# Kernel optimization log

Measured on AMD Instinct MI355X. Metric: run time of the kernel, lower is better.

## Reference

```python
import jax, jax.numpy as jnp
import numpy as np
from jax import lax

B, C_KEY, H, W = 2, 512, 48, 48
HW = H * W
TOPK = 4


def _conv(x, w, b, pad):
    # x: NCHW, w: OIHW (torch Conv2d layout)
    y = lax.conv_general_dilated(x, w, (1, 1), [(pad, pad), (pad, pad)],
                                 dimension_numbers=('NCHW', 'OIHW', 'NCHW'))
    return y + b[None, :, None, None]


def _deconv(x, w, b, stride, pad):
    # torch ConvTranspose2d weight layout (in_c, out_c, kh, kw).
    # Equivalent dilated conv: flip kernel spatially, swap in/out,
    # lhs_dilation=stride, padding=k-1-p each side.
    k = w.shape[2]
    kern = jnp.transpose(jnp.flip(w, (2, 3)), (1, 0, 2, 3))  # OIHW
    y = lax.conv_general_dilated(x, kern, (1, 1),
                                 [(k - 1 - pad, k - 1 - pad)] * 2,
                                 lhs_dilation=(stride, stride),
                                 dimension_numbers=('NCHW', 'OIHW', 'NCHW'))
    return y + b[None, :, None, None]


def setup_inputs() -> dict:
    key = jax.random.key(0)
    ks = jax.random.split(key, 32)

    def nrm(i, shape, scale=1.0):
        return jax.random.normal(ks[i], shape, jnp.float32) * scale

    def unit_key(i):
        k_ = jax.random.normal(ks[i], (B, C_KEY, H, W), jnp.float32)
        return k_ / jnp.linalg.norm(k_, axis=1, keepdims=True)

    inp = {
        'feats_s16': nrm(0, (B, 1024, H, W)),
        'feats_s8': nrm(1, (B, 512, 2 * H, 2 * W)),
        'feats_s4': nrm(2, (B, 256, 4 * H, 4 * W)),
        'key': unit_key(3),
        'init_key': unit_key(4),
        'prev_key': unit_key(5),
        'init_seg_16': jax.random.uniform(ks[6], (B, 2, H, W), jnp.float32),
        'prev_seg_16': jax.random.uniform(ks[7], (B, 2, H, W), jnp.float32),
        'mask_feats': nrm(8, (B, 256, H, W), 0.1),
        # Decoder parameters (torch layouts)
        'w_conv1': nrm(9, (256, 1024, 1, 1), 0.03), 'b_conv1': jnp.zeros((256,), jnp.float32),
        'w_blend1': nrm(10, (256, 516, 3, 3), 0.02), 'b_blend1': jnp.zeros((256,), jnp.float32),
        'w_deconv1': nrm(11, (256, 2, 4, 4), 0.02), 'b_deconv1': jnp.zeros((2,), jnp.float32),
        'w_conv2': nrm(12, (256, 512, 1, 1), 0.04), 'b_conv2': jnp.zeros((256,), jnp.float32),
        'w_blend2': nrm(13, (256, 258, 3, 3), 0.02), 'b_blend2': jnp.zeros((256,), jnp.float32),
        'w_deconv2': nrm(14, (256, 2, 4, 4), 0.02), 'b_deconv2': jnp.zeros((2,), jnp.float32),
        'w_conv3': nrm(15, (256, 256, 1, 1), 0.06), 'b_conv3': jnp.zeros((256,), jnp.float32),
        'w_blend3': nrm(16, (256, 258, 3, 3), 0.02), 'b_blend3': jnp.zeros((256,), jnp.float32),
        'w_deconv3': nrm(17, (256, 2, 6, 6), 0.02), 'b_deconv3': jnp.zeros((2,), jnp.float32),
    }
    return inp


def _forward(feats_s16, feats_s8, feats_s4, key, init_key, prev_key,
             init_seg_16, prev_seg_16, mask_feats,
             w_conv1, b_conv1, w_blend1, b_blend1, w_deconv1, b_deconv1,
             w_conv2, b_conv2, w_blend2, b_blend2, w_deconv2, b_deconv2,
             w_conv3, b_conv3, w_blend3, b_blend3, w_deconv3, b_deconv3):
    relu = jax.nn.relu
    Bn, _, Hh, Ww = key.shape
    HWn = Hh * Ww

    kf = key.reshape(Bn, -1, HWn)
    # cosine similarities mapped to [0,1]; p = ref pixel, q = query pixel
    global_sim = (jnp.einsum('bcp,bcq->bpq', init_key.reshape(Bn, -1, HWn), kf) + 1.0) * 0.5
    local_sim = (jnp.einsum('bcp,bcq->bpq', prev_key.reshape(Bn, -1, HWn), kf) + 1.0) * 0.5

    def global_score(seg_ch):  # seg_ch: (B,H,W)
        s = global_sim * seg_ch.reshape(Bn, HWn, 1)
        return jnp.max(s, axis=1)  # (B,HW)

    def local_score(seg_ch):
        s = local_sim * seg_ch.reshape(Bn, HWn, 1)  # (B,HW,HW)
        cut = lax.top_k(s, TOPK)[0][..., -1:]       # kth-largest along key dim
        mn = jnp.min(s, axis=2, keepdims=True)
        s = jnp.where(s < cut, mn, s)               # threshold masking
        return jnp.max(s, axis=1)                   # (B,HW)

    matching_score = jnp.stack([
        global_score(init_seg_16[:, 0]),
        global_score(init_seg_16[:, 1]),
        local_score(prev_seg_16[:, 0]),
        local_score(prev_seg_16[:, 1]),
    ], axis=1).reshape(Bn, 4, Hh, Ww)

    # Decoder
    x = jnp.concatenate([relu(_conv(feats_s16, w_conv1, b_conv1, 0)),
                         matching_score, mask_feats], axis=1)
    s8 = _deconv(relu(_conv(x, w_blend1, b_blend1, 1)), w_deconv1, b_deconv1, 2, 1)
    x = jnp.concatenate([relu(_conv(feats_s8, w_conv2, b_conv2, 0)), s8], axis=1)
    s4 = _deconv(relu(_conv(x, w_blend2, b_blend2, 1)), w_deconv2, b_deconv2, 2, 1)
    x = jnp.concatenate([relu(_conv(feats_s4, w_conv3, b_conv3, 0)), s4], axis=1)
    final_score = _deconv(relu(_conv(x, w_blend3, b_blend3, 1)), w_deconv3, b_deconv3, 4, 1)
    return final_score


def reference(feats_s16, feats_s8, feats_s4, key, init_key, prev_key,
              init_seg_16, prev_seg_16, mask_feats,
              w_conv1, b_conv1, w_blend1, b_blend1, w_deconv1, b_deconv1,
              w_conv2, b_conv2, w_blend2, b_blend2, w_deconv2, b_deconv2,
              w_conv3, b_conv3, w_blend3, b_blend3, w_deconv3, b_deconv3):
    return _forward(feats_s16, feats_s8, feats_s4, key, init_key, prev_key,
                    init_seg_16, prev_seg_16, mask_feats,
                    w_conv1, b_conv1, w_blend1, b_blend1, w_deconv1, b_deconv1,
                    w_conv2, b_conv2, w_blend2, b_blend2, w_deconv2, b_deconv2,
                    w_conv3, b_conv3, w_blend3, b_blend3, w_deconv3, b_deconv3)
```

## Files before the change

kernel.cpp:

```cpp
#include <hip/hip_runtime.h>
#include <cstdio>

typedef unsigned short u16;
typedef __attribute__((ext_vector_type(4))) float f32x4;
typedef __attribute__((ext_vector_type(8))) short s16x8;
typedef __attribute__((ext_vector_type(4))) unsigned short u16x4;

#define DEV static __device__ __forceinline__

DEV float bf2f(u16 u) { union { unsigned int i; float f; } v; v.i = ((unsigned int)u) << 16; return v.f; }
DEV u16 f2bf(float f) {
  unsigned int x = __float_as_uint(f);
  unsigned int r = (x + 0x7fffu + ((x >> 16) & 1u)) >> 16;
  return (u16)r;
}

typedef const __attribute__((address_space(1))) unsigned int* gptr_t;
typedef __attribute__((address_space(3))) unsigned int* lptr_t;
DEV void gl16(const u16* g, u16* l) {
  __builtin_amdgcn_global_load_lds((gptr_t)g, (lptr_t)l, 16, 0, 0);
}

__global__ __launch_bounds__(256) void trans_key(const float* __restrict__ X,
    u16* __restrict__ Y)
{
  __shared__ u16 t[64][72];
  const int tid = threadIdx.x;
  const int n0 = blockIdx.x * 64, k0 = blockIdx.y * 64, b = blockIdx.z;
  const float* Xb = X + (size_t)b * 512 * 2304;
  const int nl = tid & 63, kr = tid >> 6;
#pragma unroll
  for (int kk = 0; kk < 16; ++kk) {
    int kl = kr + kk * 4;
    t[kl][nl] = f2bf(Xb[(size_t)(k0 + kl) * 2304 + n0 + nl]);
  }
  __syncthreads();
  const int nr = tid >> 2, kb = (tid & 3) * 16;
  u16* yp = Y + (size_t)b * 2304 * 512 + (size_t)(n0 + nr) * 512 + k0 + kb;
#pragma unroll
  for (int i = 0; i < 4; ++i) {
    u16x4 v;
#pragma unroll
    for (int e = 0; e < 4; ++e) v[e] = t[kb + i * 4 + e][nr];
    *(u16x4*)&yp[i * 4] = v;
  }
}

__global__ __launch_bounds__(256) void sim_gemm_128(const u16* __restrict__ AT,
    const u16* __restrict__ BT, u16* __restrict__ out)
{
  __shared__ alignas(16) u16 Al[2][8][64][8];
  __shared__ alignas(16) u16 Bl[2][8][64][8];
  const int tid = threadIdx.x;
  const int lane = tid & 63, wv = tid >> 6;
  const int fr = lane & 15, kq = lane >> 4;
  const int wr = wv >> 1, wc = wv & 1;
  const int n0 = blockIdx.x * 128, m0 = blockIdx.y * 128, b = blockIdx.z;
  const u16* Ab = AT + (size_t)b * 2304 * 512;
  const u16* Bb = BT + (size_t)b * 2304 * 512;
  const int ar0 = m0 + wv * 16 + fr, ar1 = m0 + (wv + 4) * 16 + fr;
  const int br0 = n0 + wv * 16 + fr, br1 = n0 + (wv + 4) * 16 + fr;
  f32x4 acc[4][4];
#pragma unroll
  for (int p = 0; p < 4; ++p)
#pragma unroll
    for (int j = 0; j < 4; ++j) acc[p][j] = (f32x4){0, 0, 0, 0};
  auto ISSUE = [&](int buf, int s) {
    const int k0 = s * 32 + kq * 8;
    gl16(&Ab[(size_t)ar0 * 512 + k0], &Al[buf][wv][0][0]);
    gl16(&Ab[(size_t)ar1 * 512 + k0], &Al[buf][wv + 4][0][0]);
    gl16(&Bb[(size_t)br0 * 512 + k0], &Bl[buf][wv][0][0]);
    gl16(&Bb[(size_t)br1 * 512 + k0], &Bl[buf][wv + 4][0][0]);
  };
  ISSUE(0, 0);
  __syncthreads();
  const int NS = 512 / 32;
  for (int s = 0; s < NS; ++s) {
    const int cur = s & 1;
    if (s + 1 < NS) ISSUE(cur ^ 1, s + 1);
    s16x8 bf[4], af[4];
#pragma unroll
    for (int j = 0; j < 4; ++j) bf[j] = *(const s16x8*)&Bl[cur][wc * 4 + j][lane][0];
#pragma unroll
    for (int p = 0; p < 4; ++p) af[p] = *(const s16x8*)&Al[cur][wr * 4 + p][lane][0];
#pragma unroll
    for (int p = 0; p < 4; ++p)
#pragma unroll
      for (int j = 0; j < 4; ++j)
        acc[p][j] = __builtin_amdgcn_mfma_f32_16x16x32_bf16(af[p], bf[j], acc[p][j], 0, 0, 0);
    __syncthreads();
  }
  const int col = lane & 15, rg = (lane >> 4) * 4;
#pragma unroll
  for (int p = 0; p < 4; ++p)
#pragma unroll
    for (int j = 0; j < 4; ++j)
#pragma unroll
      for (int r = 0; r < 4; ++r) {
        int pr = m0 + (wr * 4 + p) * 16 + rg + r;
        int q = n0 + (wc * 4 + j) * 16 + col;
        out[((size_t)b * 2304 + pr) * 2304 + q] = f2bf((acc[p][j][r] + 1.0f) * 0.5f);
      }
}

__global__ __launch_bounds__(256) void rowstats(const u16* __restrict__ simL,
    float* __restrict__ cutv, float* __restrict__ mnv)
{
  const int row = blockIdx.x;
  const int tid = threadIdx.x;
  const u16* r = simL + (size_t)row * 2304;
  float t0 = -1e30f, t1 = -1e30f, t2 = -1e30f, t3 = -1e30f, mn = 1e30f;
  for (int i = tid; i < 2304; i += 256) {
    float v = bf2f(r[i]);
    mn = fminf(mn, v);
    if (v > t3) {
      if (v > t2) { t3 = t2; if (v > t1) { t2 = t1; if (v > t0) { t1 = t0; t0 = v; } else t1 = v; } else t2 = v; }
      else t3 = v;
    }
  }
  __shared__ float s4[256][4];
  __shared__ float smv[256];
  s4[tid][0] = t0; s4[tid][1] = t1; s4[tid][2] = t2; s4[tid][3] = t3;
  smv[tid] = mn;
  __syncthreads();
  for (int s = 128; s > 0; s >>= 1) {
    if (tid < s) {
      float a0 = s4[tid][0], a1 = s4[tid][1], a2 = s4[tid][2], a3 = s4[tid][3];
      float b0 = s4[tid + s][0], b1 = s4[tid + s][1], b2 = s4[tid + s][2], b3 = s4[tid + s][3];
      float m0 = fmaxf(a0, b3), m1 = fmaxf(a1, b2), m2 = fmaxf(a2, b1), m3 = fmaxf(a3, b0);
      float c0 = fmaxf(m0, m2), c2 = fminf(m0, m2), c1 = fmaxf(m1, m3), c3 = fminf(m1, m3);
      s4[tid][0] = fmaxf(c0, c1); s4[tid][1] = fminf(c0, c1);
      s4[tid][2] = fmaxf(c2, c3); s4[tid][3] = fminf(c2, c3);
      smv[tid] = fminf(smv[tid], smv[tid + s]);
    }
    __syncthreads();
  }
  if (tid == 0) { cutv[row] = s4[0][3]; mnv[row] = smv[0]; }
}

__global__ __launch_bounds__(256) void zero_f(float* __restrict__ p, int n)
{
  int i = blockIdx.x * 256 + threadIdx.x;
  if (i < n) p[i] = 0.0f;
}

__global__ __launch_bounds__(256) void zero_u16v(u16* __restrict__ p, long n4)
{
  long i = (long)blockIdx.x * 256 + threadIdx.x;
  const long stride = (long)gridDim.x * 256;
  const uint2 z = {0u, 0u};
  for (; i < n4; i += stride) ((uint2*)p)[i] = z;
}

__global__ __launch_bounds__(256) void score_global(const u16* __restrict__ sim,
    const float* __restrict__ seg, float* __restrict__ msc, int chBase)
{
  const int b = blockIdx.z;
  const int q = blockIdx.x * 256 + threadIdx.x;
  const int p0 = blockIdx.y * 128;
  const u16* sp = sim + ((size_t)b * 2304 + p0) * 2304 + q;
  const float* sg = seg + (size_t)b * 2 * 2304;
  float m0 = 0.0f, m1 = 0.0f;
  for (int p = 0; p < 128; ++p) {
    float sv = bf2f(sp[(size_t)p * 2304]);
    float s0 = sg[p0 + p];
    float s1 = sg[2304 + p0 + p];
    m0 = fmaxf(m0, sv * s0);
    m1 = fmaxf(m1, sv * s1);
  }
  atomicMax((int*)&msc[((size_t)b * 4 + chBase) * 2304 + q], __float_as_int(m0));
  atomicMax((int*)&msc[((size_t)b * 4 + chBase + 1) * 2304 + q], __float_as_int(m1));
}

__global__ __launch_bounds__(256) void score_local(const u16* __restrict__ sim,
    const float* __restrict__ seg, const float* __restrict__ cutv,
    const float* __restrict__ mnv, float* __restrict__ msc, int chBase)
{
  const int b = blockIdx.z;
  const int q = blockIdx.x * 256 + threadIdx.x;
  const int p0 = blockIdx.y * 128;
  const u16* sp = sim + ((size_t)b * 2304 + p0) * 2304 + q;
  const float* sg = seg + (size_t)b * 2 * 2304;
  const float* cu = cutv + (size_t)b * 2304 + p0;
  const float* ml = mnv + (size_t)b * 2304 + p0;
  float m0 = 0.0f, m1 = 0.0f;
  for (int p = 0; p < 128; ++p) {
    float sv = bf2f(sp[(size_t)p * 2304]);
    float cut = cu[p], mnr = ml[p];
    float mv = (sv < cut) ? mnr : sv;
    float s0 = sg[p0 + p];
    float s1 = sg[2304 + p0 + p];
    m0 = fmaxf(m0, mv * s0);
    m1 = fmaxf(m1, mv * s1);
  }
  atomicMax((int*)&msc[((size_t)b * 4 + chBase) * 2304 + q], __float_as_int(m0));
  atomicMax((int*)&msc[((size_t)b * 4 + chBase + 1) * 2304 + q], __float_as_int(m1));
}

__global__ __launch_bounds__(256) void fill_scores(const float* __restrict__ msc,
    u16* __restrict__ x1)
{
  int idx = blockIdx.x * 256 + threadIdx.x;
  if (idx >= 2 * 2304) return;
  int b = idx / 2304, q = idx % 2304;
  int py = q / 48, px = q % 48;
  u16x4 v;
#pragma unroll
  for (int c = 0; c < 4; ++c) v[c] = f2bf(msc[((size_t)b * 4 + c) * 2304 + q]);
  *(u16x4*)&x1[((size_t)b * 2500 + (py + 1) * 50 + px + 1) * 544 + 256] = v;
}

__global__ __launch_bounds__(256) void copy_mask(const float* __restrict__ mask,
    u16* __restrict__ x1)
{
  int idx = blockIdx.x * 256 + threadIdx.x;
  if (idx >= 2 * 256 * 2304) return;
  int b = idx / (256 * 2304);
  int r = idx % (256 * 2304);
  int c = r / 2304, q = r % 2304;
  int py = q / 48, px = q % 48;
  x1[((size_t)b * 2500 + (py + 1) * 50 + px + 1) * 544 + 260 + c] = f2bf(mask[idx]);
}

__global__ __launch_bounds__(256) void repack(const float* __restrict__ w,
    u16* __restrict__ wr, int IC, int ICp)
{
  int idx = blockIdx.x * 256 + threadIdx.x;
  int total = 9 * 256 * ICp;
  if (idx >= total) return;
  int ic = idx % ICp;
  int oc = (idx / ICp) % 256;
  int tap = idx / (ICp * 256);
  wr[idx] = (ic < IC) ? f2bf(w[((size_t)oc * IC + ic) * 9 + tap]) : (u16)0;
}

__global__ __launch_bounds__(256) void repack_w(const float* __restrict__ w,
    u16* __restrict__ o, int n)
{
  int i = blockIdx.x * 256 + threadIdx.x;
  if (i < n) o[i] = f2bf(w[i]);
}

__global__ __launch_bounds__(256) void repack_dec(const float* __restrict__ w,
    u16* __restrict__ wr, int S, int KSZ, int MT)
{
  int idx = blockIdx.x * 256 + threadIdx.x;
  int total = MT * 16 * 1024;
  if (idx >= total) return;
  int m = idx >> 10, k = idx & 1023;
  int oc = m & 1, ph = m >> 1;
  int tap = k >> 8, ic = k & 255;
  int dy = tap >> 1, dx = tap & 1;
  float val = 0.0f;
  if (ph < S * S) {
    int ry = ph / S, rx = ph % S;
    int ky = ry + S * dy, kx = rx + S * dx;
    if (ky < KSZ && kx < KSZ)
      val = w[((size_t)(ic * 2 + oc) * KSZ + ky) * KSZ + kx];
  }
  wr[idx] = f2bf(val);
}

template<int MB>
__global__ __launch_bounds__(256) void conv1x1_gl(const float* __restrict__ X,
    const u16* __restrict__ Wb, const float* __restrict__ bias,
    u16* __restrict__ Y, int K, int WD, int Cp)
{
  const int N = WD * WD;
  const int P = WD + 2, HWp = P * P;
  constexpr int SUB = MB / 16, SPW = SUB / 4;
  __shared__ alignas(16) u16 Al[2][SUB][64][8];
  __shared__ alignas(16) u16 Bl[2][4][64][8];
  const int tid = threadIdx.x;
  const int n0 = blockIdx.x * 64, m0 = blockIdx.y * MB, b = blockIdx.z;
  const int lane = tid & 63, wv = tid >> 6;
  const int fr = lane & 15, kq = lane >> 4;
  const float* Xb = X + (size_t)b * K * N;
  const int bpix = n0 + wv * 16 + fr;
  f32x4 acc[SPW][4];
#pragma unroll
  for (int p = 0; p < SPW; ++p)
#pragma unroll
    for (int j = 0; j < 4; ++j) acc[p][j] = (f32x4){0, 0, 0, 0};
  s16x8 bN;
  auto ISSUEA = [&](int buf, int s) {
    const int k0 = s * 32 + kq * 8;
#pragma unroll
    for (int p = 0; p < SPW; ++p)
      gl16(&Wb[(size_t)(m0 + (wv * SPW + p) * 16 + fr) * K + k0],
           &Al[buf][wv * SPW + p][0][0]);
  };
  auto LDB = [&](int s) {
    const int k0 = s * 32;
#pragma unroll
    for (int i = 0; i < 8; ++i)
      bN[i] = (short)f2bf(Xb[(size_t)(k0 + kq * 8 + i) * N + bpix]);
  };
  ISSUEA(0, 0); LDB(0);
  *(s16x8*)&Bl[0][wv][lane][0] = bN;
  __syncthreads();
  const int NS = K / 32;
  for (int s = 0; s < NS; ++s) {
    const int cur = s & 1;
    const bool more = (s + 1) < NS;
    if (more) { ISSUEA(cur ^ 1, s + 1); LDB(s + 1); }
    s16x8 bf[4];
#pragma unroll
    for (int j = 0; j < 4; ++j) bf[j] = *(const s16x8*)&Bl[cur][j][lane][0];
#pragma unroll
    for (int p = 0; p < SPW; ++p) {
      s16x8 af = *(const s16x8*)&Al[cur][wv * SPW + p][lane][0];
#pragma unroll
      for (int j = 0; j < 4; ++j)
        acc[p][j] = __builtin_amdgcn_mfma_f32_16x16x32_bf16(af, bf[j], acc[p][j], 0, 0, 0);
    }
    if (more) *(s16x8*)&Bl[cur ^ 1][wv][lane][0] = bN;
    __syncthreads();
  }
  const int col = lane & 15, rg = (lane >> 4) * 4;
#pragma unroll
  for (int j = 0; j < 4; ++j) {
    const int nn = n0 + j * 16 + col;
    const int py = nn / WD, px = nn % WD;
    const size_t rowb = ((size_t)b * HWp + (py + 1) * P + px + 1) * Cp;
#pragma unroll
    for (int p = 0; p < SPW; ++p) {
      const int oc0 = m0 + (wv * SPW + p) * 16 + rg;
      u16x4 v;
#pragma unroll
      for (int r = 0; r < 4; ++r)
        v[r] = f2bf(fmaxf(acc[p][j][r] + bias[oc0 + r], 0.0f));
      *(u16x4*)&Y[rowb + oc0] = v;
    }
  }
}

template<int WD, int MB>
__global__ __launch_bounds__(256) void blend3x3_gl(const u16* __restrict__ X,
    const u16* __restrict__ Wr, const float* __restrict__ bias,
    u16* __restrict__ Y, int ICp)
{
  constexpr int P = WD + 2, HWp = P * P, HW = WD * WD;
  constexpr int SUB = MB / 16, SPW = SUB / 4;
  __shared__ alignas(16) u16 Al[2][SUB][64][8];
  __shared__ alignas(16) u16 Bl[2][4][64][8];
  const int tid = threadIdx.x;
  const int lane = tid & 63, wv = tid >> 6;
  const int fr = lane & 15, kq = lane >> 4;
  const int n0 = blockIdx.x * 64, m0 = blockIdx.y * MB, b = blockIdx.z;
  const int KS = ICp / 32, NS = 9 * KS;
  const u16* Xb = X + (size_t)b * HWp * ICp;
  const int bpix = n0 + wv * 16 + fr;
  const int brow = (bpix / WD + 1) * P + (bpix % WD) + 1;
  f32x4 acc[SPW][4];
#pragma unroll
  for (int p = 0; p < SPW; ++p)
#pragma unroll
    for (int j = 0; j < 4; ++j) acc[p][j] = (f32x4){0, 0, 0, 0};
  auto ISSUE = [&](int buf, int s) {
    const int tap = s / KS, k0 = (s - tap * KS) * 32 + kq * 8;
    const int dy = tap / 3 - 1, dx = tap % 3 - 1;
    gl16(&Xb[(size_t)(brow + dy * P + dx) * ICp + k0], &Bl[buf][wv][0][0]);
    const u16* wt = Wr + (size_t)tap * 256 * ICp + k0;
#pragma unroll
    for (int p = 0; p < SPW; ++p)
      gl16(&wt[(size_t)(m0 + (wv * SPW + p) * 16 + fr) * ICp],
           &Al[buf][wv * SPW + p][0][0]);
  };
  ISSUE(0, 0);
  __syncthreads();
  for (int s = 0; s < NS; ++s) {
    const int cur = s & 1;
    if (s + 1 < NS) ISSUE(cur ^ 1, s + 1);
    s16x8 bf[4];
#pragma unroll
    for (int j = 0; j < 4; ++j) bf[j] = *(const s16x8*)&Bl[cur][j][lane][0];
#pragma unroll
    for (int p = 0; p < SPW; ++p) {
      s16x8 af = *(const s16x8*)&Al[cur][wv * SPW + p][lane][0];
#pragma unroll
      for (int j = 0; j < 4; ++j)
        acc[p][j] = __builtin_amdgcn_mfma_f32_16x16x32_bf16(af, bf[j], acc[p][j], 0, 0, 0);
    }
    __syncthreads();
  }
  const int col = lane & 15, rg = (lane >> 4) * 4;
#pragma unroll
  for (int j = 0; j < 4; ++j) {
    const int nn = n0 + j * 16 + col;
    const size_t rowb = ((size_t)b * HW + nn) * 256;
#pragma unroll
    for (int p = 0; p < SPW; ++p) {
      const int oc0 = m0 + (wv * SPW + p) * 16 + rg;
      u16x4 v;
#pragma unroll
      for (int r = 0; r < 4; ++r)
        v[r] = f2bf(fmaxf(acc[p][j][r] + bias[oc0 + r], 0.0f));
      *(u16x4*)&Y[rowb + oc0] = v;
    }
  }
}

template<int WD, int MB>
__global__ __launch_bounds__(256) void blend3x3_bk64(const u16* __restrict__ X,
    const u16* __restrict__ Wr, const float* __restrict__ bias,
    u16* __restrict__ Y, int ICp)
{
  constexpr int P = WD + 2, HWp = P * P, HW = WD * WD;
  constexpr int SUB = MB / 16, SPW = SUB / 4;
  __shared__ alignas(16) u16 Al[2][2][SUB][64][8];
  __shared__ alignas(16) u16 Bl[2][2][4][64][8];
  const int tid = threadIdx.x;
  const int lane = tid & 63, wv = tid >> 6;
  const int fr = lane & 15, kq = lane >> 4;
  const int n0 = blockIdx.x * 64, m0 = blockIdx.y * MB, b = blockIdx.z;
  const int KS = ICp / 32, NS = 9 * KS;
  const int NPAIR = (NS + 1) / 2;
  const u16* Xb = X + (size_t)b * HWp * ICp;
  const int bpix = n0 + wv * 16 + fr;
  const int brow = (bpix / WD + 1) * P + (bpix % WD) + 1;
  f32x4 acc[SPW][4];
#pragma unroll
  for (int p = 0; p < SPW; ++p)
#pragma unroll
    for (int j = 0; j < 4; ++j) acc[p][j] = (f32x4){0, 0, 0, 0};
  auto ISSUE = [&](int buf, int sp) {
#pragma unroll
    for (int h = 0; h < 2; ++h) {
      const int s = sp * 2 + h;
      if (s >= NS) break;
      const int tap = s / KS, k0 = (s - tap * KS) * 32 + kq * 8;
      const int dy = tap / 3 - 1, dx = tap % 3 - 1;
      gl16(&Xb[(size_t)(brow + dy * P + dx) * ICp + k0], &Bl[buf][h][wv][0][0]);
      const u16* wt = Wr + (size_t)tap * 256 * ICp + k0;
#pragma unroll
      for (int p = 0; p < SPW; ++p)
        gl16(&wt[(size_t)(m0 + (wv * SPW + p) * 16 + fr) * ICp],
             &Al[buf][h][wv * SPW + p][0][0]);
    }
  };
  ISSUE(0, 0);
  __syncthreads();
  for (int sp = 0; sp < NPAIR; ++sp) {
    const int cur = sp & 1;
    if (sp + 1 < NPAIR) ISSUE(cur ^ 1, sp + 1);
#pragma unroll
    for (int h = 0; h < 2; ++h) {
      if (sp * 2 + h >= NS) break;
      s16x8 bf[4];
#pragma unroll
      for (int j = 0; j < 4; ++j) bf[j] = *(const s16x8*)&Bl[cur][h][j][lane][0];
#pragma unroll
      for (int p = 0; p < SPW; ++p) {
        s16x8 af = *(const s16x8*)&Al[cur][h][wv * SPW + p][lane][0];
#pragma unroll
        for (int j = 0; j < 4; ++j)
          acc[p][j] = __builtin_amdgcn_mfma_f32_16x16x32_bf16(af, bf[j], acc[p][j], 0, 0, 0);
      }
    }
    __syncthreads();
  }
  const int col = lane & 15, rg = (lane >> 4) * 4;
#pragma unroll
  for (int j = 0; j < 4; ++j) {
    const int nn = n0 + j * 16 + col;
    const size_t rowb = ((size_t)b * HW + nn) * 256;
#pragma unroll
    for (int p = 0; p < SPW; ++p) {
      const int oc0 = m0 + (wv * SPW + p) * 16 + rg;
      u16x4 v;
#pragma unroll
      for (int r = 0; r < 4; ++r)
        v[r] = f2bf(fmaxf(acc[p][j][r] + bias[oc0 + r], 0.0f));
      *(u16x4*)&Y[rowb + oc0] = v;
    }
  }
}

template<int S, int WIN, int MT, bool F32OUT>
__global__ __launch_bounds__(256) void deconv_dir(const u16* __restrict__ X,
    const u16* __restrict__ Wr, const float* __restrict__ bias,
    void* __restrict__ Yout, int Cp, int coff)
{
  constexpr int NP1 = WIN + 1;
  constexpr int Np = NP1 * NP1;
  constexpr int WO = S * WIN;
  constexpr int HWin = WIN * WIN;
  constexpr int Pout = WO + 2, HWpo = Pout * Pout;
  const int tid = threadIdx.x;
  const int lane = tid & 63, wv = tid >> 6;
  const int fr = lane & 15, kq = lane >> 4;
  const int n0 = blockIdx.x * 64, b = blockIdx.y;
  const u16* Xb = X + (size_t)b * HWin * 256 + kq * 8;
  const int pixn = n0 + wv * 16 + fr;
  const int t_y = pixn / NP1, t_x = pixn % NP1;
  f32x4 acc[MT];
#pragma unroll
  for (int mt = 0; mt < MT; ++mt) acc[mt] = (f32x4){0, 0, 0, 0};
#pragma unroll
  for (int tap = 0; tap < 4; ++tap) {
    const int dy = tap >> 1, dx = tap & 1;
    const int iy = t_y - dy, ix = t_x - dx;
    const bool vsp = (pixn < Np) && ((unsigned)iy < (unsigned)WIN) && ((unsigned)ix < (unsigned)WIN);
    const u16* bpt = Xb + (size_t)(vsp ? iy * WIN + ix : 0) * 256;
    for (int kk = 0; kk < 256; kk += 32) {
      s16x8 bf = *(const s16x8*)(bpt + kk);
      if (!vsp) {
#pragma unroll
        for (int i = 0; i < 8; ++i) bf[i] = 0;
      }
#pragma unroll
      for (int mt = 0; mt < MT; ++mt) {
        s16x8 af = *(const s16x8*)&Wr[(size_t)(mt * 16 + fr) * 1024 + tap * 256 + kk + kq * 8];
        acc[mt] = __builtin_amdgcn_mfma_f32_16x16x32_bf16(af, bf, acc[mt], 0, 0, 0);
      }
    }
  }
  const int col = lane & 15, rg = (lane >> 4) * 4;
  const int nn = n0 + wv * 16 + col;
  if (nn >= Np) return;
  const int oty = nn / NP1, otx = nn % NP1;
#pragma unroll
  for (int mt = 0; mt < MT; ++mt) {
#pragma unroll
    for (int r = 0; r < 4; ++r) {
      int m = mt * 16 + rg + r;
      int ph = m >> 1, oc = m & 1;
      if (ph >= S * S) continue;
      int ry = ph / S, rx = ph % S;
      int oy = S * oty + ry - 1, ox = S * otx + rx - 1;
      if ((unsigned)oy >= (unsigned)WO || (unsigned)ox >= (unsigned)WO) continue;
      float v = acc[mt][r] + bias[oc];
      if (F32OUT)
        ((float*)Yout)[((size_t)b * 2 + oc) * WO * WO + (size_t)oy * WO + ox] = v;
      else
        ((u16*)Yout)[((size_t)b * HWpo + (oy + 1) * Pout + ox + 1) * Cp + coff + oc] = f2bf(v);
    }
  }
}

extern "C" void kernel_launch(void* const* d_in, const int* in_sizes, int n_in,
                              void* d_out, int out_size, void* d_ws, size_t ws_size,
                              hipStream_t stream)
{
  const float* feats_s16 = (const float*)d_in[0];
  const float* feats_s8  = (const float*)d_in[1];
  const float* feats_s4  = (const float*)d_in[2];
  const float* key       = (const float*)d_in[3];
  const float* init_key  = (const float*)d_in[4];
  const float* prev_key  = (const float*)d_in[5];
  const float* init_seg  = (const float*)d_in[6];
  const float* prev_seg  = (const float*)d_in[7];
  const float* mask_f    = (const float*)d_in[8];
  const float* w_conv1 = (const float*)d_in[9];  const float* b_conv1 = (const float*)d_in[10];
  const float* w_blend1= (const float*)d_in[11]; const float* b_blend1= (const float*)d_in[12];
  const float* w_dec1  = (const float*)d_in[13]; const float* b_dec1  = (const float*)d_in[14];
  const float* w_conv2 = (const float*)d_in[15]; const float* b_conv2 = (const float*)d_in[16];
  const float* w_blend2= (const float*)d_in[17]; const float* b_blend2= (const float*)d_in[18];
  const float* w_dec2  = (const float*)d_in[19]; const float* b_dec2  = (const float*)d_in[20];
  const float* w_conv3 = (const float*)d_in[21]; const float* b_conv3 = (const float*)d_in[22];
  const float* w_blend3= (const float*)d_in[23]; const float* b_blend3= (const float*)d_in[24];
  const float* w_dec3  = (const float*)d_in[25]; const float* b_dec3  = (const float*)d_in[26];

  char* ws = (char*)d_ws;
  size_t o = 0;
  auto take = [&](size_t n) { size_t r = o; o += (n + 255) & ~(size_t)255; return r; };
  u16* simG = (u16*)(ws + take((size_t)2 * 2304 * 2304 * 2));
  u16* simL = (u16*)(ws + take((size_t)2 * 2304 * 2304 * 2));
  float* cutv = (float*)(ws + take((size_t)2 * 2304 * 4));
  float* mnv  = (float*)(ws + take((size_t)2 * 2304 * 4));
  float* msc  = (float*)(ws + take((size_t)2 * 4 * 2304 * 4));
  u16* x1  = (u16*)(ws + take((size_t)2 * 2500 * 544 * 2));
  u16* b1o = (u16*)(ws + take((size_t)2 * 2304 * 256 * 2));
  u16* x2  = (u16*)(ws + take((size_t)2 * 9604 * 288 * 2));
  u16* b2o = (u16*)(ws + take((size_t)2 * 9216 * 256 * 2));
  u16* x3  = (u16*)(ws + take((size_t)2 * 37636 * 288 * 2));
  u16* b3o = (u16*)(ws + take((size_t)2 * 36864 * 256 * 2));
  u16* wr1 = (u16*)(ws + take((size_t)9 * 256 * 544 * 2));
  u16* wr2 = (u16*)(ws + take((size_t)9 * 256 * 288 * 2));
  u16* wr3 = (u16*)(ws + take((size_t)9 * 256 * 288 * 2));
  u16* wd1r = (u16*)(ws + take((size_t)16 * 1024 * 2));
  u16* wd2r = (u16*)(ws + take((size_t)16 * 1024 * 2));
  u16* wd3r = (u16*)(ws + take((size_t)32 * 1024 * 2));
  u16* keyT = (u16*)(ws + take((size_t)2 * 2304 * 512 * 2));
  u16* ikT  = (u16*)(ws + take((size_t)2 * 2304 * 512 * 2));
  u16* pkT  = (u16*)(ws + take((size_t)2 * 2304 * 512 * 2));
  u16* wc1b = (u16*)(ws + take((size_t)256 * 1024 * 2));
  u16* wc2b = (u16*)(ws + take((size_t)256 * 512 * 2));
  u16* wc3b = (u16*)(ws + take((size_t)256 * 256 * 2));
  if (o > ws_size) {
    fprintf(stderr, "kernel_launch: ws too small: need %zu, have %zu\n", o, ws_size);
    return;
  }

  zero_u16v<<<dim3(2048), 256, 0, stream>>>(x1, (long)2 * 2500 * 544 / 4);
  zero_u16v<<<dim3(2048), 256, 0, stream>>>(x2, (long)2 * 9604 * 288 / 4);
  zero_u16v<<<dim3(2048), 256, 0, stream>>>(x3, (long)2 * 37636 * 288 / 4);
  repack<<<dim3((9 * 256 * 544 + 255) / 256), 256, 0, stream>>>(w_blend1, wr1, 516, 544);
  repack<<<dim3((9 * 256 * 288 + 255) / 256), 256, 0, stream>>>(w_blend2, wr2, 258, 288);
  repack<<<dim3((9 * 256 * 288 + 255) / 256), 256, 0, stream>>>(w_blend3, wr3, 258, 288);
  repack_dec<<<dim3(64), 256, 0, stream>>>(w_dec1, wd1r, 2, 4, 1);
  repack_dec<<<dim3(64), 256, 0, stream>>>(w_dec2, wd2r, 2, 4, 1);
  repack_dec<<<dim3(128), 256, 0, stream>>>(w_dec3, wd3r, 4, 6, 2);
  repack_w<<<dim3(1024), 256, 0, stream>>>(w_conv1, wc1b, 256 * 1024);
  repack_w<<<dim3(512), 256, 0, stream>>>(w_conv2, wc2b, 256 * 512);
  repack_w<<<dim3(256), 256, 0, stream>>>(w_conv3, wc3b, 256 * 256);
  trans_key<<<dim3(36, 8, 2), 256, 0, stream>>>(key, keyT);
  trans_key<<<dim3(36, 8, 2), 256, 0, stream>>>(init_key, ikT);
  trans_key<<<dim3(36, 8, 2), 256, 0, stream>>>(prev_key, pkT);

  sim_gemm_128<<<dim3(18, 18, 2), 256, 0, stream>>>(ikT, keyT, simG);
  sim_gemm_128<<<dim3(18, 18, 2), 256, 0, stream>>>(pkT, keyT, simL);

  rowstats<<<dim3(2 * 2304), 256, 0, stream>>>(simL, cutv, mnv);
  zero_f<<<dim3(72), 256, 0, stream>>>(msc, 2 * 4 * 2304);
  score_global<<<dim3(9, 18, 2), 256, 0, stream>>>(simG, init_seg, msc, 0);
  score_local<<<dim3(9, 18, 2), 256, 0, stream>>>(simL, prev_seg, cutv, mnv, msc, 2);

  conv1x1_gl<64><<<dim3(36, 4, 2), 256, 0, stream>>>(feats_s16, wc1b, b_conv1, x1, 1024, 48, 544);
  fill_scores<<<dim3(18), 256, 0, stream>>>(msc, x1);
  copy_mask<<<dim3(4608), 256, 0, stream>>>(mask_f, x1);
  blend3x3_bk64<48, 64><<<dim3(36, 4, 2), 256, 0, stream>>>(x1, wr1, b_blend1, b1o, 544);
  deconv_dir<2, 48, 1, false><<<dim3((49 * 49 + 63) / 64, 2), 256, 0, stream>>>(
      b1o, wd1r, b_dec1, x2, 288, 256);

  conv1x1_gl<128><<<dim3(144, 2, 2), 256, 0, stream>>>(feats_s8, wc2b, b_conv2, x2, 512, 96, 288);
  blend3x3_bk64<96, 128><<<dim3(144, 2, 2), 256, 0, stream>>>(x2, wr2, b_blend2, b2o, 288);
  deconv_dir<2, 96, 1, false><<<dim3((97 * 97 + 63) / 64, 2), 256, 0, stream>>>(
      b2o, wd2r, b_dec2, x3, 288, 256);

  conv1x1_gl<256><<<dim3(576, 1, 2), 256, 0, stream>>>(feats_s4, wc3b, b_conv3, x3, 256, 192, 288);
  blend3x3_gl<192, 256><<<dim3(576, 1, 2), 256, 0, stream>>>(x3, wr3, b_blend3, b3o, 288);
  deconv_dir<4, 192, 2, true><<<dim3((193 * 193 + 63) / 64, 2), 256, 0, stream>>>(
      b3o, wd3r, b_dec3, d_out, 2, 0);
}
```

Baseline: 712.7 us.

## Add triple-buffered blend3x3 pipeline with explicit vmcnt waits and split M tiles

New measurement: 788.1 us. 10.6% more time.

```diff
diff --git a/kernel.cpp b/kernel.cpp
--- a/kernel.cpp
+++ b/kernel.cpp
@@ -20,6 +20,12 @@
 DEV void gl16(const u16* g, u16* l) {
   __builtin_amdgcn_global_load_lds((gptr_t)g, (lptr_t)l, 16, 0, 0);
 }
+
+#define VM6 asm volatile("s_waitcnt vmcnt(6)" ::: "memory")
+#define VM3 asm volatile("s_waitcnt vmcnt(3)" ::: "memory")
+#define VM0 asm volatile("s_waitcnt vmcnt(0)" ::: "memory")
+#define BARRIER __builtin_amdgcn_s_barrier()
+#define SCHED0 __builtin_amdgcn_sched_barrier(0)
 
 __global__ __launch_bounds__(256) void trans_key(const float* __restrict__ X,
     u16* __restrict__ Y)
@@ -336,72 +342,6 @@
 }
 
 template<int WD, int MB>
-__global__ __launch_bounds__(256) void blend3x3_gl(const u16* __restrict__ X,
-    const u16* __restrict__ Wr, const float* __restrict__ bias,
-    u16* __restrict__ Y, int ICp)
-{
-  constexpr int P = WD + 2, HWp = P * P, HW = WD * WD;
-  constexpr int SUB = MB / 16, SPW = SUB / 4;
-  __shared__ alignas(16) u16 Al[2][SUB][64][8];
-  __shared__ alignas(16) u16 Bl[2][4][64][8];
-  const int tid = threadIdx.x;
-  const int lane = tid & 63, wv = tid >> 6;
-  const int fr = lane & 15, kq = lane >> 4;
-  const int n0 = blockIdx.x * 64, m0 = blockIdx.y * MB, b = blockIdx.z;
-  const int KS = ICp / 32, NS = 9 * KS;
-  const u16* Xb = X + (size_t)b * HWp * ICp;
-  const int bpix = n0 + wv * 16 + fr;
-  const int brow = (bpix / WD + 1) * P + (bpix % WD) + 1;
-  f32x4 acc[SPW][4];
-#pragma unroll
-  for (int p = 0; p < SPW; ++p)
-#pragma unroll
-    for (int j = 0; j < 4; ++j) acc[p][j] = (f32x4){0, 0, 0, 0};
-  auto ISSUE = [&](int buf, int s) {
-    const int tap = s / KS, k0 = (s - tap * KS) * 32 + kq * 8;
-    const int dy = tap / 3 - 1, dx = tap % 3 - 1;
-    gl16(&Xb[(size_t)(brow + dy * P + dx) * ICp + k0], &Bl[buf][wv][0][0]);
-    const u16* wt = Wr + (size_t)tap * 256 * ICp + k0;
-#pragma unroll
-    for (int p = 0; p < SPW; ++p)
-      gl16(&wt[(size_t)(m0 + (wv * SPW + p) * 16 + fr) * ICp],
-           &Al[buf][wv * SPW + p][0][0]);
-  };
-  ISSUE(0, 0);
-  __syncthreads();
-  for (int s = 0; s < NS; ++s) {
-    const int cur = s & 1;
-    if (s + 1 < NS) ISSUE(cur ^ 1, s + 1);
-    s16x8 bf[4];
-#pragma unroll
-    for (int j = 0; j < 4; ++j) bf[j] = *(const s16x8*)&Bl[cur][j][lane][0];
-#pragma unroll
-    for (int p = 0; p < SPW; ++p) {
-      s16x8 af = *(const s16x8*)&Al[cur][wv * SPW + p][lane][0];
-#pragma unroll
-      for (int j = 0; j < 4; ++j)
-        acc[p][j] = __builtin_amdgcn_mfma_f32_16x16x32_bf16(af, bf[j], acc[p][j], 0, 0, 0);
-    }
-    __syncthreads();
-  }
-  const int col = lane & 15, rg = (lane >> 4) * 4;
-#pragma unroll
-  for (int j = 0; j < 4; ++j) {
-    const int nn = n0 + j * 16 + col;
-    const size_t rowb = ((size_t)b * HW + nn) * 256;
-#pragma unroll
-    for (int p = 0; p < SPW; ++p) {
-      const int oc0 = m0 + (wv * SPW + p) * 16 + rg;
-      u16x4 v;
-#pragma unroll
-      for (int r = 0; r < 4; ++r)
-        v[r] = f2bf(fmaxf(acc[p][j][r] + bias[oc0 + r], 0.0f));
-      *(u16x4*)&Y[rowb + oc0] = v;
-    }
-  }
-}
-
-template<int WD, int MB>
 __global__ __launch_bounds__(256) void blend3x3_bk64(const u16* __restrict__ X,
     const u16* __restrict__ Wr, const float* __restrict__ bias,
     u16* __restrict__ Y, int ICp)
@@ -459,6 +399,93 @@
       }
     }
     __syncthreads();
+  }
+  const int col = lane & 15, rg = (lane >> 4) * 4;
+#pragma unroll
+  for (int j = 0; j < 4; ++j) {
+    const int nn = n0 + j * 16 + col;
+    const size_t rowb = ((size_t)b * HW + nn) * 256;
+#pragma unroll
+    for (int p = 0; p < SPW; ++p) {
+      const int oc0 = m0 + (wv * SPW + p) * 16 + rg;
+      u16x4 v;
+#pragma unroll
+      for (int r = 0; r < 4; ++r)
+        v[r] = f2bf(fmaxf(acc[p][j][r] + bias[oc0 + r], 0.0f));
+      *(u16x4*)&Y[rowb + oc0] = v;
+    }
+  }
+}
+
+template<int WD, int MB>
+__global__ __launch_bounds__(256) void blend3x3_pipe(const u16* __restrict__ X,
+    const u16* __restrict__ Wr, const float* __restrict__ bias,
+    u16* __restrict__ Y, int ICp)
+{
+  constexpr int P = WD + 2, HWp = P * P, HW = WD * WD;
+  constexpr int SUB = MB / 16, SPW = SUB / 4;
+  __shared__ alignas(16) u16 Al[3][2][SUB][64][8];
+  __shared__ alignas(16) u16 Bl[3][2][4][64][8];
+  const int tid = threadIdx.x;
+  const int lane = tid & 63, wv = tid >> 6;
+  const int fr = lane & 15, kq = lane >> 4;
+  const int n0 = blockIdx.x * 64, m0 = blockIdx.y * MB, b = blockIdx.z;
+  const int KS = ICp / 32, NS = 9 * KS;
+  const int NPAIR = (NS + 1) / 2;
+  const u16* Xb = X + (size_t)b * HWp * ICp;
+  const int bpix = n0 + wv * 16 + fr;
+  const int brow = (bpix / WD + 1) * P + (bpix % WD) + 1;
+  f32x4 acc[SPW][4];
+#pragma unroll
+  for (int p = 0; p < SPW; ++p)
+#pragma unroll
+    for (int j = 0; j < 4; ++j) acc[p][j] = (f32x4){0, 0, 0, 0};
+  auto ISSUE = [&](int buf, int sp) {
+#pragma unroll
+    for (int h = 0; h < 2; ++h) {
+      const int s = sp * 2 + h;
+      if (s >= NS) break;
+      const int tap = s / KS, k0 = (s - tap * KS) * 32 + kq * 8;
+      const int dy = tap / 3 - 1, dx = tap % 3 - 1;
+      gl16(&Xb[(size_t)(brow + dy * P + dx) * ICp + k0], &Bl[buf][h][wv][0][0]);
+      const u16* wt = Wr + (size_t)tap * 256 * ICp + k0;
+#pragma unroll
+      for (int p = 0; p < SPW; ++p)
+        gl16(&wt[(size_t)(m0 + (wv * SPW + p) * 16 + fr) * ICp],
+             &Al[buf][h][wv * SPW + p][0][0]);
+    }
+  };
+  auto nloads = [&](int sp) -> int {
+    if (sp >= NPAIR) return 0;
+    int rem = NS - sp * 2;
+    return rem >= 2 ? 3 * 2 : 3;
+  };
+  ISSUE(0, 0);
+  if (NPAIR > 1) ISSUE(1, 1);
+  for (int sp = 0; sp < NPAIR; ++sp) {
+    const int cur = sp % 3;
+    const int allow = nloads(sp + 1);
+    if (allow >= 6) { VM6; } else if (allow >= 3) { VM3; } else { VM0; }
+    BARRIER;
+    SCHED0;
+    if (sp + 2 < NPAIR) ISSUE((sp + 2) % 3, sp + 2);
+#pragma unroll
+    for (int h = 0; h < 2; ++h) {
+      if (sp * 2 + h >= NS) break;
+      s16x8 bf[4];
+#pragma unroll
+      for (int j = 0; j < 4; ++j) bf[j] = *(const s16x8*)&Bl[cur][h][j][lane][0];
+#pragma unroll
+      for (int p = 0; p < SPW; ++p) {
+        s16x8 af = *(const s16x8*)&Al[cur][h][wv * SPW + p][lane][0];
+#pragma unroll
+        for (int j = 0; j < 4; ++j)
+          acc[p][j] = __builtin_amdgcn_mfma_f32_16x16x32_bf16(af, bf[j], acc[p][j], 0, 0, 0);
+      }
+    }
+    asm volatile("s_waitcnt lgkmcnt(0)" ::: "memory");
+    BARRIER;
+    SCHED0;
   }
   const int col = lane & 15, rg = (lane >> 4) * 4;
 #pragma unroll
@@ -625,12 +652,12 @@
       b1o, wd1r, b_dec1, x2, 288, 256);
 
   conv1x1_gl<128><<<dim3(144, 2, 2), 256, 0, stream>>>(feats_s8, wc2b, b_conv2, x2, 512, 96, 288);
-  blend3x3_bk64<96, 128><<<dim3(144, 2, 2), 256, 0, stream>>>(x2, wr2, b_blend2, b2o, 288);
+  blend3x3_pipe<96, 128><<<dim3(144, 2, 2), 256, 0, stream>>>(x2, wr2, b_blend2, b2o, 288);
   deconv_dir<2, 96, 1, false><<<dim3((97 * 97 + 63) / 64, 2), 256, 0, stream>>>(
       b2o, wd2r, b_dec2, x3, 288, 256);
 
-  conv1x1_gl<256><<<dim3(576, 1, 2), 256, 0, stream>>>(feats_s4, wc3b, b_conv3, x3, 256, 192, 288);
-  blend3x3_gl<192, 256><<<dim3(576, 1, 2), 256, 0, stream>>>(x3, wr3, b_blend3, b3o, 288);
+  conv1x1_gl<128><<<dim3(576, 2, 2), 256, 0, stream>>>(feats_s4, wc3b, b_conv3, x3, 256, 192, 288);
+  blend3x3_pipe<192, 128><<<dim3(576, 2, 2), 256, 0, stream>>>(x3, wr3, b_blend3, b3o, 288);
   deconv_dir<4, 192, 2, true><<<dim3((193 * 193 + 63) / 64, 2), 256, 0, stream>>>(
       b3o, wd3r, b_dec3, d_out, 2, 0);
 }
```
